# Performance work log

Measured on AMD Instinct MI355X. Metric: run time of the kernel, lower is better.

Reference implementation:

```python
import jax, jax.numpy as jnp
import numpy as np

B, T, C = 4, 1024, 1024
H = 16
HD = C // H          # head_size = 64
FF = 4 * C           # 4096


def setup_inputs() -> dict:
    key = jax.random.key(0)
    ks = jax.random.split(key, 12)
    s = 0.02
    return {
        "x": jax.random.normal(ks[0], (B, T, C), dtype=jnp.float32),
        "ln1_g": jnp.ones((C,), jnp.float32),
        "ln1_b": jnp.zeros((C,), jnp.float32),
        "ln2_g": jnp.ones((C,), jnp.float32),
        "ln2_b": jnp.zeros((C,), jnp.float32),
        "Wq": jax.random.normal(ks[1], (H, C, HD), jnp.float32) * s,
        "Wk": jax.random.normal(ks[2], (H, C, HD), jnp.float32) * s,
        "Wv": jax.random.normal(ks[3], (H, C, HD), jnp.float32) * s,
        "Wproj": jax.random.normal(ks[4], (C, C), jnp.float32) * s,
        "bproj": jnp.zeros((C,), jnp.float32),
        "W1": jax.random.normal(ks[5], (C, FF), jnp.float32) * s,
        "b1": jnp.zeros((FF,), jnp.float32),
        "W2": jax.random.normal(ks[6], (FF, C), jnp.float32) * s,
        "b2": jnp.zeros((C,), jnp.float32),
    }


def _layernorm(x, g, b, eps=1e-5):
    mu = jnp.mean(x, axis=-1, keepdims=True)
    var = jnp.var(x, axis=-1, keepdims=True)
    return (x - mu) * jax.lax.rsqrt(var + eps) * g + b


def _attention(xn, Wq, Wk, Wv, Wproj, bproj):
    # per-head projections, vectorized over heads: [B,T,C] x [H,C,HD] -> [B,H,T,HD]
    q = jnp.einsum("btc,hcd->bhtd", xn, Wq)
    k = jnp.einsum("btc,hcd->bhtd", xn, Wk)
    v = jnp.einsum("btc,hcd->bhtd", xn, Wv)
    scale = HD ** (-0.5)
    w = jnp.einsum("bhtd,bhsd->bhts", q, k) * scale  # [B,H,T,T]
    tq = jnp.arange(xn.shape[1])
    causal = tq[:, None] >= tq[None, :]               # tril mask [T,T]
    w = jnp.where(causal, w, -jnp.inf)
    w = jax.nn.softmax(w, axis=-1)
    att = jnp.einsum("bhts,bhsd->bhtd", w, v)         # [B,H,T,HD]
    # concat heads in order -> [B,T,H*HD]
    att = jnp.transpose(att, (0, 2, 1, 3)).reshape(xn.shape[0], xn.shape[1], -1)
    return att @ Wproj + bproj


def _ffn(xn, W1, b1, W2, b2):
    h = jax.nn.gelu(xn @ W1 + b1, approximate=False)  # torch nn.GELU default = exact
    return h @ W2 + b2


def reference(x, ln1_g, ln1_b, ln2_g, ln2_b, Wq, Wk, Wv, Wproj, bproj, W1, b1, W2, b2):
    x = x + _attention(_layernorm(x, ln1_g, ln1_b), Wq, Wk, Wv, Wproj, bproj)
    x = x + _ffn(_layernorm(x, ln2_g, ln2_b), W1, b1, W2, b2)
    return x
```

## Files before the change

kernel.cpp:

```cpp
#include <hip/hip_runtime.h>
#include <hip/hip_bf16.h>
#include <math.h>

#define Bn 4
#define Tn 1024
#define Cn 1024
#define Hn 16
#define HDn 64
#define FFn 4096

typedef unsigned short ushort_t;
typedef __attribute__((ext_vector_type(8))) short bf16x8;
typedef __attribute__((ext_vector_type(4))) float f32x4;

__device__ __forceinline__ ushort_t f2bf(float f) {
  unsigned u = __float_as_uint(f);
  u += 0x7fffu + ((u >> 16) & 1u);
  return (ushort_t)(u >> 16);
}

__device__ __forceinline__ void gload_lds16(const void* g, void* l) {
  __builtin_amdgcn_global_load_lds(
      (const __attribute__((address_space(1))) void*)g,
      (__attribute__((address_space(3))) void*)l, 16, 0, 0);
}

__global__ __launch_bounds__(256) void ln_kernel(const float* __restrict__ x,
                                                 const float* __restrict__ g,
                                                 const float* __restrict__ b,
                                                 ushort_t* __restrict__ out) {
  int row = blockIdx.x;
  const float4 v = reinterpret_cast<const float4*>(x + (size_t)row * Cn)[threadIdx.x];
  float s  = v.x + v.y + v.z + v.w;
  float s2 = v.x * v.x + v.y * v.y + v.z * v.z + v.w * v.w;
  for (int m = 1; m < 64; m <<= 1) {
    s  += __shfl_xor(s, m, 64);
    s2 += __shfl_xor(s2, m, 64);
  }
  __shared__ float ls[4], ls2[4];
  int wid = threadIdx.x >> 6;
  if ((threadIdx.x & 63) == 0) { ls[wid] = s; ls2[wid] = s2; }
  __syncthreads();
  s  = ls[0] + ls[1] + ls[2] + ls[3];
  s2 = ls2[0] + ls2[1] + ls2[2] + ls2[3];
  const float mean = s * (1.0f / Cn);
  const float var  = s2 * (1.0f / Cn) - mean * mean;
  const float rstd = rsqrtf(var + 1e-5f);
  const float4 gv = reinterpret_cast<const float4*>(g)[threadIdx.x];
  const float4 bv = reinterpret_cast<const float4*>(b)[threadIdx.x];
  float4 o;
  o.x = (v.x - mean) * rstd * gv.x + bv.x;
  o.y = (v.y - mean) * rstd * gv.y + bv.y;
  o.z = (v.z - mean) * rstd * gv.z + bv.z;
  o.w = (v.w - mean) * rstd * gv.w + bv.w;
  uint2 pk;
  pk.x = (unsigned)f2bf(o.x) | ((unsigned)f2bf(o.y) << 16);
  pk.y = (unsigned)f2bf(o.z) | ((unsigned)f2bf(o.w) << 16);
  reinterpret_cast<uint2*>(out + (size_t)row * Cn)[threadIdx.x] = pk;
}

__global__ __launch_bounds__(256) void transpose_f2b(const float* __restrict__ in,
                                                     ushort_t* __restrict__ out,
                                                     int K, int N) {
  __shared__ float t[32][33];
  const int n0 = blockIdx.x * 32, k0 = blockIdx.y * 32;
  const int tx = threadIdx.x & 31, ty = threadIdx.x >> 5;
#pragma unroll
  for (int i = 0; i < 4; ++i)
    t[ty + i * 8][tx] = in[(size_t)(k0 + ty + i * 8) * N + n0 + tx];
  __syncthreads();
#pragma unroll
  for (int i = 0; i < 4; ++i)
    out[(size_t)(n0 + ty + i * 8) * K + k0 + tx] = f2bf(t[tx][ty + i * 8]);
}

__global__ __launch_bounds__(256) void repack_qkv_bf(const float* __restrict__ Wq,
                                                     const float* __restrict__ Wk,
                                                     const float* __restrict__ Wv,
                                                     ushort_t* __restrict__ out) {
  __shared__ float t[32][33];
  const int z = blockIdx.z;
  const int ti = z >> 4, h = z & 15;
  const float* in = (ti == 0 ? Wq : (ti == 1 ? Wk : Wv)) + (size_t)h * Cn * HDn;
  ushort_t* o = out + (size_t)(ti * Cn + h * HDn) * Cn;
  const int n0 = blockIdx.x * 32, k0 = blockIdx.y * 32;
  const int tx = threadIdx.x & 31, ty = threadIdx.x >> 5;
#pragma unroll
  for (int i = 0; i < 4; ++i)
    t[ty + i * 8][tx] = in[(size_t)(k0 + ty + i * 8) * HDn + n0 + tx];
  __syncthreads();
#pragma unroll
  for (int i = 0; i < 4; ++i)
    o[(size_t)(n0 + ty + i * 8) * Cn + k0 + tx] = f2bf(t[tx][ty + i * 8]);
}

__global__ __launch_bounds__(256) void vtrans(const ushort_t* __restrict__ qkv,
                                              ushort_t* __restrict__ vT) {
  __shared__ ushort_t t[32][34];
  const int t0 = blockIdx.x * 32;
  const int d0 = blockIdx.y * 32;
  const int bh = blockIdx.z;
  const int b = bh >> 4, h = bh & 15;
  const int tx = threadIdx.x & 31, ty = threadIdx.x >> 5;
#pragma unroll
  for (int i = 0; i < 4; ++i)
    t[ty + i * 8][tx] = qkv[(size_t)(b * Tn + t0 + ty + i * 8) * (3 * Cn) +
                            2 * Cn + h * HDn + d0 + tx];
  __syncthreads();
#pragma unroll
  for (int i = 0; i < 4; ++i)
    vT[(size_t)(bh * HDn + d0 + ty + i * 8) * Tn + t0 + tx] = t[tx][ty + i * 8];
}

__global__ __launch_bounds__(256) void gemm_bt(const ushort_t* __restrict__ A,
                                               const ushort_t* __restrict__ Bt,
                                               const float* __restrict__ bias,
                                               const float* __restrict__ res,
                                               float* __restrict__ Cf,
                                               ushort_t* __restrict__ Cb,
                                               int M, int N, int K, int act) {
  __shared__ ushort_t As[128 * 32];
  __shared__ ushort_t Bs[128 * 32];
  const int tid = threadIdx.x;
  const int w = tid >> 6, lane = tid & 63;
  const int n0 = blockIdx.x * 128, m0 = blockIdx.y * 128;
  const int wr = w >> 1, wc = w & 1;
  const int lr = lane & 15, lg = lane >> 4;

  f32x4 acc[4][4];
  const f32x4 zero = {0.f, 0.f, 0.f, 0.f};
#pragma unroll
  for (int i = 0; i < 4; ++i)
#pragma unroll
    for (int j = 0; j < 4; ++j) acc[i][j] = zero;

  const int srow = lane >> 2;
  const int skc  = (lane & 3) * 8;
  const ushort_t* Ag = A  + (size_t)(m0 + w * 32 + srow) * K + skc;
  const ushort_t* Bg = Bt + (size_t)(n0 + w * 32 + srow) * K + skc;
  ushort_t* lA0 = &As[(w * 32) * 32];
  ushort_t* lA1 = &As[(w * 32 + 16) * 32];
  ushort_t* lB0 = &Bs[(w * 32) * 32];
  ushort_t* lB1 = &Bs[(w * 32 + 16) * 32];

  for (int k0 = 0; k0 < K; k0 += 32) {
    gload_lds16(Ag + k0, lA0);
    gload_lds16(Ag + (size_t)16 * K + k0, lA1);
    gload_lds16(Bg + k0, lB0);
    gload_lds16(Bg + (size_t)16 * K + k0, lB1);
    __syncthreads();
    bf16x8 af[4], bf_[4];
#pragma unroll
    for (int m = 0; m < 4; ++m)
      af[m] = *reinterpret_cast<const bf16x8*>(&As[(wr * 64 + m * 16 + lr) * 32 + lg * 8]);
#pragma unroll
    for (int n = 0; n < 4; ++n)
      bf_[n] = *reinterpret_cast<const bf16x8*>(&Bs[(wc * 64 + n * 16 + lr) * 32 + lg * 8]);
#pragma unroll
    for (int m = 0; m < 4; ++m)
#pragma unroll
      for (int n = 0; n < 4; ++n)
        acc[m][n] = __builtin_amdgcn_mfma_f32_16x16x32_bf16(af[m], bf_[n], acc[m][n], 0, 0, 0);
    __syncthreads();
  }

#pragma unroll
  for (int m = 0; m < 4; ++m) {
    const int rowb = m0 + wr * 64 + m * 16 + lg * 4;
#pragma unroll
    for (int n = 0; n < 4; ++n) {
      const int col = n0 + wc * 64 + n * 16 + lr;
      const float bb = bias ? bias[col] : 0.0f;
      f32x4 v = acc[m][n];
#pragma unroll
      for (int r = 0; r < 4; ++r) {
        float y = v[r] + bb;
        if (act == 1) y = 0.5f * y * (1.0f + erff(y * 0.70710678118654752f));
        if (res) y += res[(size_t)(rowb + r) * N + col];
        if (Cb) Cb[(size_t)(rowb + r) * N + col] = f2bf(y);
        else    Cf[(size_t)(rowb + r) * N + col] = y;
      }
    }
  }
}

__global__ __launch_bounds__(256) void attn_mfma(const ushort_t* __restrict__ qkv,
                                                 const ushort_t* __restrict__ vT,
                                                 ushort_t* __restrict__ out) {
  const int qt = blockIdx.x, h = blockIdx.y, b = blockIdx.z;
  const int tid = threadIdx.x;
  const int w = tid >> 6;
  const int lane = tid & 63;
  const int lr = lane & 15, lg = lane >> 4;
  const int q0 = qt * 64;
  const int bh = b * Hn + h;

  __shared__ ushort_t Ks[64 * 64];
  __shared__ ushort_t Vts[64 * 64];
  __shared__ ushort_t Ps[64 * 64];

  bf16x8 qf[2];
  {
    const ushort_t* qp = qkv + (size_t)(b * Tn + q0 + w * 16 + lr) * (3 * Cn) + h * HDn;
    qf[0] = *reinterpret_cast<const bf16x8*>(qp + lg * 8);
    qf[1] = *reinterpret_cast<const bf16x8*>(qp + 32 + lg * 8);
  }

  f32x4 acc[4];
  const f32x4 fzero = {0.f, 0.f, 0.f, 0.f};
  acc[0] = acc[1] = acc[2] = acc[3] = fzero;
  float m_[4] = {-1e30f, -1e30f, -1e30f, -1e30f};
  float l_[4] = {0.f, 0.f, 0.f, 0.f};

  const int srow = tid >> 3;
  const int sc   = (tid & 7) * 8;

  for (int kt = 0; kt <= qt; ++kt) {
    const int s0 = kt * 64;
#pragma unroll
    for (int p = 0; p < 2; ++p) {
      const int row = srow + p * 32;
      const uint4 kv = *reinterpret_cast<const uint4*>(
          qkv + (size_t)(b * Tn + s0 + row) * (3 * Cn) + Cn + h * HDn + sc);
      *reinterpret_cast<uint4*>(&Ks[row * 64 + (sc ^ ((row & 7) << 3))]) = kv;
      const uint4 vv = *reinterpret_cast<const uint4*>(
          vT + (size_t)(bh * HDn + row) * Tn + s0 + sc);
      *reinterpret_cast<uint4*>(&Vts[row * 64 + (sc ^ ((row & 7) << 3))]) = vv;
    }
    __syncthreads();

    f32x4 sf[4];
    sf[0] = sf[1] = sf[2] = sf[3] = fzero;
#pragma unroll
    for (int n = 0; n < 4; ++n) {
      const int krow = n * 16 + lr;
#pragma unroll
      for (int c = 0; c < 2; ++c) {
        const bf16x8 kf = *reinterpret_cast<const bf16x8*>(
            &Ks[krow * 64 + ((c * 32 + lg * 8) ^ ((krow & 7) << 3))]);
        sf[n] = __builtin_amdgcn_mfma_f32_16x16x32_bf16(qf[c], kf, sf[n], 0, 0, 0);
      }
    }

    const bool diag = (kt == qt);
#pragma unroll
    for (int r = 0; r < 4; ++r) {
      const int qg = q0 + w * 16 + lg * 4 + r;
      float mx = -1e30f;
#pragma unroll
      for (int n = 0; n < 4; ++n) {
        float s = sf[n][r] * 0.125f;
        if (diag && (s0 + n * 16 + lr) > qg) s = -1e30f;
        sf[n][r] = s;
        mx = fmaxf(mx, s);
      }
      mx = fmaxf(mx, __shfl_xor(mx, 1));
      mx = fmaxf(mx, __shfl_xor(mx, 2));
      mx = fmaxf(mx, __shfl_xor(mx, 4));
      mx = fmaxf(mx, __shfl_xor(mx, 8));
      const float mn = fmaxf(m_[r], mx);
      const float sfac = __expf(m_[r] - mn);
      m_[r] = mn;
      float ls = 0.f;
#pragma unroll
      for (int n = 0; n < 4; ++n) {
        const float p = __expf(sf[n][r] - mn);
        sf[n][r] = p;
        ls += p;
      }
      ls += __shfl_xor(ls, 1);
      ls += __shfl_xor(ls, 2);
      ls += __shfl_xor(ls, 4);
      ls += __shfl_xor(ls, 8);
      l_[r] = l_[r] * sfac + ls;
#pragma unroll
      for (int n = 0; n < 4; ++n) acc[n][r] *= sfac;
      const int prow = w * 16 + lg * 4 + r;
#pragma unroll
      for (int n = 0; n < 4; ++n)
        Ps[prow * 64 + ((n * 16 + lr) ^ ((prow & 7) << 3))] = f2bf(sf[n][r]);
    }

#pragma unroll
    for (int sb = 0; sb < 2; ++sb) {
      const int prow = w * 16 + lr;
      const bf16x8 pf = *reinterpret_cast<const bf16x8*>(
          &Ps[prow * 64 + ((sb * 32 + lg * 8) ^ ((prow & 7) << 3))]);
#pragma unroll
      for (int nf = 0; nf < 4; ++nf) {
        const int vrow = nf * 16 + lr;
        const bf16x8 vf = *reinterpret_cast<const bf16x8*>(
            &Vts[vrow * 64 + ((sb * 32 + lg * 8) ^ ((vrow & 7) << 3))]);
        acc[nf] = __builtin_amdgcn_mfma_f32_16x16x32_bf16(pf, vf, acc[nf], 0, 0, 0);
      }
    }
    __syncthreads();
  }

#pragma unroll
  for (int r = 0; r < 4; ++r) {
    const float inv = 1.0f / l_[r];
    const int qg = q0 + w * 16 + lg * 4 + r;
#pragma unroll
    for (int nf = 0; nf < 4; ++nf)
      out[(size_t)(b * Tn + qg) * Cn + h * HDn + nf * 16 + lr] = f2bf(acc[nf][r] * inv);
  }
}

extern "C" void kernel_launch(void* const* d_in, const int* in_sizes, int n_in,
                              void* d_out, int out_size, void* d_ws, size_t ws_size,
                              hipStream_t stream) {
  const float* x      = (const float*)d_in[0];
  const float* ln1_g  = (const float*)d_in[1];
  const float* ln1_b  = (const float*)d_in[2];
  const float* ln2_g  = (const float*)d_in[3];
  const float* ln2_b  = (const float*)d_in[4];
  const float* Wq     = (const float*)d_in[5];
  const float* Wk     = (const float*)d_in[6];
  const float* Wv     = (const float*)d_in[7];
  const float* Wproj  = (const float*)d_in[8];
  const float* bproj  = (const float*)d_in[9];
  const float* W1     = (const float*)d_in[10];
  const float* b1     = (const float*)d_in[11];
  const float* W2     = (const float*)d_in[12];
  const float* b2     = (const float*)d_in[13];
  float* out = (float*)d_out;

  char* wsb = (char*)d_ws;
  ushort_t* xn_bf   = (ushort_t*)(wsb);
  ushort_t* attn_bf = (ushort_t*)(wsb + ((size_t)8  << 20));
  float*    x2      = (float*)  (wsb + ((size_t)16 << 20));
  ushort_t* qkv_bf  = (ushort_t*)(wsb + ((size_t)32 << 20));
  ushort_t* vTb     = (ushort_t*)(wsb + ((size_t)56 << 20));
  ushort_t* hbuf    = (ushort_t*)(wsb + ((size_t)32 << 20));
  ushort_t* wqkv_t  = (ushort_t*)(wsb + ((size_t)64 << 20));
  ushort_t* wproj_t = (ushort_t*)(wsb + ((size_t)70 << 20));
  ushort_t* w1_t    = (ushort_t*)(wsb + ((size_t)72 << 20));
  ushort_t* w2_t    = (ushort_t*)(wsb + ((size_t)80 << 20));

  const int Mrows = Bn * Tn;

  repack_qkv_bf<<<dim3(2, 32, 48), 256, 0, stream>>>(Wq, Wk, Wv, wqkv_t);
  transpose_f2b<<<dim3(Cn / 32, Cn / 32), 256, 0, stream>>>(Wproj, wproj_t, Cn, Cn);
  transpose_f2b<<<dim3(FFn / 32, Cn / 32), 256, 0, stream>>>(W1, w1_t, Cn, FFn);
  transpose_f2b<<<dim3(Cn / 32, FFn / 32), 256, 0, stream>>>(W2, w2_t, FFn, Cn);

  ln_kernel<<<Mrows, 256, 0, stream>>>(x, ln1_g, ln1_b, xn_bf);

  gemm_bt<<<dim3(3 * Cn / 128, Mrows / 128), 256, 0, stream>>>(
      xn_bf, wqkv_t, nullptr, nullptr, nullptr, qkv_bf, Mrows, 3 * Cn, Cn, 0);

  vtrans<<<dim3(Tn / 32, HDn / 32, Bn * Hn), 256, 0, stream>>>(qkv_bf, vTb);

  attn_mfma<<<dim3(Tn / 64, Hn, Bn), 256, 0, stream>>>(qkv_bf, vTb, attn_bf);

  gemm_bt<<<dim3(Cn / 128, Mrows / 128), 256, 0, stream>>>(
      attn_bf, wproj_t, bproj, x, x2, nullptr, Mrows, Cn, Cn, 0);

  ln_kernel<<<Mrows, 256, 0, stream>>>(x2, ln2_g, ln2_b, xn_bf);

  gemm_bt<<<dim3(FFn / 128, Mrows / 128), 256, 0, stream>>>(
      xn_bf, w1_t, b1, nullptr, nullptr, hbuf, Mrows, FFn, Cn, 1);

  gemm_bt<<<dim3(Cn / 128, Mrows / 128), 256, 0, stream>>>(
      hbuf, w2_t, b2, x2, out, nullptr, Mrows, Cn, FFn, 0);
}
```

Before: 471.3 us.

## Double-buffer GEMM LDS tiles and use 64-row tiles for N=1024 GEMMs

The GEMM kernel now keeps two LDS buffers and issues the global-to-LDS loads for the next K tile before computing the current one, dropping one barrier per iteration. The intent is to overlap memory latency with MFMA work. The kernel is also templated on tile height, and the projection and FFN2 GEMMs (N=1024) use 64x128 tiles so more blocks are launched and more CUs are filled. The risks are extra LDS per block, lower per-block reuse for the smaller tile, and a possible race: the next-tile asynchronous LDS writes are issued without waiting for outstanding loads before the barrier.

```diff
diff --git a/kernel.cpp b/kernel.cpp
--- a/kernel.cpp
+++ b/kernel.cpp
@@ -112,6 +112,7 @@
     vT[(size_t)(bh * HDn + d0 + ty + i * 8) * Tn + t0 + tx] = t[tx][ty + i * 8];
 }
 
+template <int BM>
 __global__ __launch_bounds__(256) void gemm_bt(const ushort_t* __restrict__ A,
                                                const ushort_t* __restrict__ Bt,
                                                const float* __restrict__ bias,
@@ -119,57 +120,69 @@
                                                float* __restrict__ Cf,
                                                ushort_t* __restrict__ Cb,
                                                int M, int N, int K, int act) {
-  __shared__ ushort_t As[128 * 32];
-  __shared__ ushort_t Bs[128 * 32];
+  constexpr int FN = (BM == 128) ? 4 : 2;
+  __shared__ ushort_t As[2][BM * 32];
+  __shared__ ushort_t Bs[2][128 * 32];
   const int tid = threadIdx.x;
   const int w = tid >> 6, lane = tid & 63;
-  const int n0 = blockIdx.x * 128, m0 = blockIdx.y * 128;
-  const int wr = w >> 1, wc = w & 1;
+  const int n0 = blockIdx.x * 128, m0 = blockIdx.y * BM;
+  const int woffM = (BM == 128) ? (w >> 1) * 64 : 0;
+  const int woffN = (BM == 128) ? (w & 1) * 64 : w * 32;
   const int lr = lane & 15, lg = lane >> 4;
 
-  f32x4 acc[4][4];
+  f32x4 acc[4][FN];
   const f32x4 zero = {0.f, 0.f, 0.f, 0.f};
 #pragma unroll
   for (int i = 0; i < 4; ++i)
 #pragma unroll
-    for (int j = 0; j < 4; ++j) acc[i][j] = zero;
+    for (int j = 0; j < FN; ++j) acc[i][j] = zero;
 
   const int srow = lane >> 2;
   const int skc  = (lane & 3) * 8;
-  const ushort_t* Ag = A  + (size_t)(m0 + w * 32 + srow) * K + skc;
+  const int arow0 = (BM == 128) ? (w * 32) : (w * 16);
+  const ushort_t* Ag = A  + (size_t)(m0 + arow0 + srow) * K + skc;
   const ushort_t* Bg = Bt + (size_t)(n0 + w * 32 + srow) * K + skc;
-  ushort_t* lA0 = &As[(w * 32) * 32];
-  ushort_t* lA1 = &As[(w * 32 + 16) * 32];
-  ushort_t* lB0 = &Bs[(w * 32) * 32];
-  ushort_t* lB1 = &Bs[(w * 32 + 16) * 32];
-
-  for (int k0 = 0; k0 < K; k0 += 32) {
-    gload_lds16(Ag + k0, lA0);
-    gload_lds16(Ag + (size_t)16 * K + k0, lA1);
-    gload_lds16(Bg + k0, lB0);
-    gload_lds16(Bg + (size_t)16 * K + k0, lB1);
+
+  const int NT = K >> 5;
+
+  auto stage = [&](int buf, int k0) {
+    gload_lds16(Ag + k0, &As[buf][arow0 * 32]);
+    if (BM == 128)
+      gload_lds16(Ag + (size_t)16 * K + k0, &As[buf][(arow0 + 16) * 32]);
+    gload_lds16(Bg + k0, &Bs[buf][(w * 32) * 32]);
+    gload_lds16(Bg + (size_t)16 * K + k0, &Bs[buf][(w * 32 + 16) * 32]);
+  };
+
+  stage(0, 0);
+  __syncthreads();
+
+  int cur = 0;
+  for (int t = 0; t < NT; ++t) {
+    if (t + 1 < NT) stage(cur ^ 1, (t + 1) << 5);
+    bf16x8 af[4], bfr[FN];
+#pragma unroll
+    for (int m = 0; m < 4; ++m)
+      af[m] = *reinterpret_cast<const bf16x8*>(
+          &As[cur][(woffM + m * 16 + lr) * 32 + lg * 8]);
+#pragma unroll
+    for (int n = 0; n < FN; ++n)
+      bfr[n] = *reinterpret_cast<const bf16x8*>(
+          &Bs[cur][(woffN + n * 16 + lr) * 32 + lg * 8]);
+#pragma unroll
+    for (int m = 0; m < 4; ++m)
+#pragma unroll
+      for (int n = 0; n < FN; ++n)
+        acc[m][n] = __builtin_amdgcn_mfma_f32_16x16x32_bf16(af[m], bfr[n], acc[m][n], 0, 0, 0);
     __syncthreads();
-    bf16x8 af[4], bf_[4];
-#pragma unroll
-    for (int m = 0; m < 4; ++m)
-      af[m] = *reinterpret_cast<const bf16x8*>(&As[(wr * 64 + m * 16 + lr) * 32 + lg * 8]);
-#pragma unroll
-    for (int n = 0; n < 4; ++n)
-      bf_[n] = *reinterpret_cast<const bf16x8*>(&Bs[(wc * 64 + n * 16 + lr) * 32 + lg * 8]);
-#pragma unroll
-    for (int m = 0; m < 4; ++m)
-#pragma unroll
-      for (int n = 0; n < 4; ++n)
-        acc[m][n] = __builtin_amdgcn_mfma_f32_16x16x32_bf16(af[m], bf_[n], acc[m][n], 0, 0, 0);
-    __syncthreads();
+    cur ^= 1;
   }
 
 #pragma unroll
   for (int m = 0; m < 4; ++m) {
-    const int rowb = m0 + wr * 64 + m * 16 + lg * 4;
-#pragma unroll
-    for (int n = 0; n < 4; ++n) {
-      const int col = n0 + wc * 64 + n * 16 + lr;
+    const int rowb = m0 + woffM + m * 16 + lg * 4;
+#pragma unroll
+    for (int n = 0; n < FN; ++n) {
+      const int col = n0 + woffN + n * 16 + lr;
       const float bb = bias ? bias[col] : 0.0f;
       f32x4 v = acc[m][n];
 #pragma unroll
@@ -347,21 +360,21 @@
 
   ln_kernel<<<Mrows, 256, 0, stream>>>(x, ln1_g, ln1_b, xn_bf);
 
-  gemm_bt<<<dim3(3 * Cn / 128, Mrows / 128), 256, 0, stream>>>(
+  gemm_bt<128><<<dim3(3 * Cn / 128, Mrows / 128), 256, 0, stream>>>(
       xn_bf, wqkv_t, nullptr, nullptr, nullptr, qkv_bf, Mrows, 3 * Cn, Cn, 0);
 
   vtrans<<<dim3(Tn / 32, HDn / 32, Bn * Hn), 256, 0, stream>>>(qkv_bf, vTb);
 
   attn_mfma<<<dim3(Tn / 64, Hn, Bn), 256, 0, stream>>>(qkv_bf, vTb, attn_bf);
 
-  gemm_bt<<<dim3(Cn / 128, Mrows / 128), 256, 0, stream>>>(
+  gemm_bt<64><<<dim3(Cn / 128, Mrows / 64), 256, 0, stream>>>(
       attn_bf, wproj_t, bproj, x, x2, nullptr, Mrows, Cn, Cn, 0);
 
   ln_kernel<<<Mrows, 256, 0, stream>>>(x2, ln2_g, ln2_b, xn_bf);
 
-  gemm_bt<<<dim3(FFn / 128, Mrows / 128), 256, 0, stream>>>(
+  gemm_bt<128><<<dim3(FFn / 128, Mrows / 128), 256, 0, stream>>>(
       xn_bf, w1_t, b1, nullptr, nullptr, hbuf, Mrows, FFn, Cn, 1);
 
-  gemm_bt<<<dim3(Cn / 128, Mrows / 128), 256, 0, stream>>>(
+  gemm_bt<64><<<dim3(Cn / 128, Mrows / 64), 256, 0, stream>>>(
       hbuf, w2_t, b2, x2, out, nullptr, Mrows, Cn, FFn, 0);
 }
```

After: 411.4 us. 1.15x faster.
